# Performance work log

Hardware: AMD Instinct MI355X
Metric: run time of the kernel (lower is better)

## Reference

```python
import jax, jax.numpy as jnp
import numpy as np

B, S, D, H = 2, 2048, 2048, 16
DK = D // H
THETA = 10000.0


def setup_inputs() -> dict:
    key = jax.random.key(0)
    ks = jax.random.split(key, 5)
    scale = 0.02
    return {
        "x": jax.random.normal(ks[0], (B, S, D), dtype=jnp.float32),
        "W_Q": jax.random.normal(ks[1], (D, D), dtype=jnp.float32) * scale,
        "W_K": jax.random.normal(ks[2], (D, D), dtype=jnp.float32) * scale,
        "W_V": jax.random.normal(ks[3], (D, D), dtype=jnp.float32) * scale,
        "W_O": jax.random.normal(ks[4], (D, D), dtype=jnp.float32) * scale,
        "token_positions": jnp.arange(S, dtype=jnp.int32),
    }


def _rope(x, pos):
    # x: [B, S, H, DK]; pos: [S]. Interleaved-pair rotation (cs336 RoPE).
    half = DK // 2
    inv_freq = THETA ** (-(jnp.arange(half, dtype=jnp.float32) / half))  # [half]
    ang = pos.astype(jnp.float32)[:, None] * inv_freq[None, :]           # [S, half]
    cos = jnp.cos(ang)[None, :, None, :]                                 # [1,S,1,half]
    sin = jnp.sin(ang)[None, :, None, :]
    x1, x2 = x[..., ::2], x[..., 1::2]
    r1 = x1 * cos - x2 * sin
    r2 = x1 * sin + x2 * cos
    return jnp.stack([r1, r2], axis=-1).reshape(x.shape)


def reference(x, W_Q, W_K, W_V, W_O, token_positions):
    # QKV projections (Linear with no bias: y = x @ W^T)
    Q = (x @ W_Q.T).reshape(B, S, H, DK)
    K = (x @ W_K.T).reshape(B, S, H, DK)
    V = (x @ W_V.T).reshape(B, S, H, DK)
    Q = _rope(Q, token_positions)
    K = _rope(K, token_positions)
    scores = jnp.einsum("bqhd,bkhd->bhqk", Q, K) / jnp.sqrt(jnp.float32(DK))
    causal = jnp.tril(jnp.ones((S, S), dtype=bool))  # True = attend
    scores = jnp.where(causal[None, None], scores, -jnp.inf)
    attn = jax.nn.softmax(scores, axis=-1)
    out = jnp.einsum("bhqk,bkhd->bqhd", attn, V).reshape(B, S, D)
    return out @ W_O.T
```

## Files before the change

kernel.cpp:

```cpp
#include <hip/hip_runtime.h>
#include <hip/hip_bf16.h>
#include <cstdint>
#include <cstddef>

#define B_ 2
#define S_ 2048
#define D_ 2048
#define H_ 16
#define DK_ 128
#define M_ (B_*S_)

typedef __attribute__((ext_vector_type(8))) __bf16 bf16x8;
typedef __attribute__((ext_vector_type(4))) float f32x4;
typedef __attribute__((ext_vector_type(16))) float f32x16;

__device__ __forceinline__ unsigned short f2bf(float f) {
  union { float f; unsigned int u; } v; v.f = f;
  unsigned int r = (v.u + 0x7fffu + ((v.u >> 16) & 1u)) >> 16;
  return (unsigned short)r;
}
__device__ __forceinline__ float bf2f(unsigned short b) {
  union { unsigned int u; float f; } v; v.u = ((unsigned int)b) << 16;
  return v.f;
}

__device__ __forceinline__ void gld16(const void* g, void* l) {
  __builtin_amdgcn_global_load_lds(
      (const __attribute__((address_space(1))) unsigned int*)g,
      (__attribute__((address_space(3))) unsigned int*)l, 16, 0, 0);
}

__global__ void cvt_bf16(const float* __restrict__ src, unsigned short* __restrict__ dst, int n) {
  int i = (blockIdx.x * blockDim.x + threadIdx.x) * 4;
  if (i + 3 < n) {
    float4 v = *(const float4*)(src + i);
    dst[i+0] = f2bf(v.x); dst[i+1] = f2bf(v.y);
    dst[i+2] = f2bf(v.z); dst[i+3] = f2bf(v.w);
  }
}

template<int WRITE_BF16>
__global__ __launch_bounds__(256) void gemm_bt(const unsigned short* __restrict__ A,
                                               const unsigned short* __restrict__ W0,
                                               const unsigned short* __restrict__ W1,
                                               const unsigned short* __restrict__ W2,
                                               void* __restrict__ C0, void* __restrict__ C1,
                                               void* __restrict__ C2,
                                               int M, int N, int K) {
  __shared__ unsigned short sA[128 * 32];
  __shared__ unsigned short sB[128 * 32];
  const int z = blockIdx.z;
  const unsigned short* Bt = (z == 0) ? W0 : (z == 1) ? W1 : W2;
  void* Cout = (z == 0) ? C0 : (z == 1) ? C1 : C2;

  const int tid  = threadIdx.x;
  const int lane = tid & 63;
  const int wid  = tid >> 6;
  const int wm = wid >> 1, wn = wid & 1;
  const int quad = lane >> 4, l16 = lane & 15;
  const int bm = blockIdx.y * 128, bn = blockIdx.x * 128;
  const int srow = lane >> 2;
  const int scol = (lane & 3) * 8;

  f32x4 acc[4][4];
  #pragma unroll
  for (int i = 0; i < 4; ++i)
    #pragma unroll
    for (int j = 0; j < 4; ++j)
      acc[i][j] = (f32x4){0.f, 0.f, 0.f, 0.f};

  for (int k0 = 0; k0 < K; k0 += 32) {
    __syncthreads();
    #pragma unroll
    for (int p = 0; p < 2; ++p) {
      int row = p * 64 + wid * 16;
      gld16(A  + (size_t)(bm + row + srow) * K + k0 + scol, sA + row * 32);
      gld16(Bt + (size_t)(bn + row + srow) * K + k0 + scol, sB + row * 32);
    }
    __syncthreads();

    bf16x8 af[4], bfr[4];
    #pragma unroll
    for (int i = 0; i < 4; ++i)
      af[i] = *(const bf16x8*)(sA + (wm * 64 + i * 16 + l16) * 32 + quad * 8);
    #pragma unroll
    for (int j = 0; j < 4; ++j)
      bfr[j] = *(const bf16x8*)(sB + (wn * 64 + j * 16 + l16) * 32 + quad * 8);
    #pragma unroll
    for (int i = 0; i < 4; ++i)
      #pragma unroll
      for (int j = 0; j < 4; ++j)
        acc[i][j] = __builtin_amdgcn_mfma_f32_16x16x32_bf16(af[i], bfr[j], acc[i][j], 0, 0, 0);
  }

  #pragma unroll
  for (int i = 0; i < 4; ++i) {
    int row = bm + wm * 64 + i * 16 + quad * 4;
    #pragma unroll
    for (int j = 0; j < 4; ++j) {
      int col = bn + wn * 64 + j * 16 + l16;
      #pragma unroll
      for (int r = 0; r < 4; ++r) {
        if (WRITE_BF16)
          ((unsigned short*)Cout)[(size_t)(row + r) * N + col] = f2bf(acc[i][j][r]);
        else
          ((float*)Cout)[(size_t)(row + r) * N + col] = acc[i][j][r];
      }
    }
  }
}

__global__ void rope_kernel(unsigned short* __restrict__ Q, unsigned short* __restrict__ K,
                            const int* __restrict__ pos) {
  int idx = blockIdx.x * blockDim.x + threadIdx.x;
  int i = idx & 63;
  int h = (idx >> 6) & (H_ - 1);
  int s = (idx >> 10) & (S_ - 1);
  int b = idx >> 21;
  float p = (float)pos[s];
  float inv = expf(-(float)i * (9.210340371976184f / 64.0f));
  float ang = p * inv;
  float sn, cs;
  sincosf(ang, &sn, &cs);
  size_t base = (((size_t)b * S_ + s) * D_) + (size_t)h * DK_ + 2 * i;
  float x1 = bf2f(Q[base]), x2 = bf2f(Q[base + 1]);
  Q[base]     = f2bf(x1 * cs - x2 * sn);
  Q[base + 1] = f2bf(x1 * sn + x2 * cs);
  x1 = bf2f(K[base]); x2 = bf2f(K[base + 1]);
  K[base]     = f2bf(x1 * cs - x2 * sn);
  K[base + 1] = f2bf(x1 * sn + x2 * cs);
}

__global__ __launch_bounds__(256) void transpose_bf16(const unsigned short* __restrict__ src,
                                                      unsigned short* __restrict__ dst) {
  __shared__ unsigned short sT[64 * 64];
  const int b = blockIdx.y;
  const int tx = blockIdx.x & 31, ty = blockIdx.x >> 5;
  const size_t base = (size_t)b * 2048 * 2048;
  const int m0 = ty * 64, c0 = tx * 64;
  const int tid = threadIdx.x;
  #pragma unroll
  for (int c = 0; c < 2; ++c) {
    int idx = tid + c * 256;
    int row = idx >> 3;
    int chk = idx & 7;
    uint4 v = *(const uint4*)(src + base + (size_t)(m0 + row) * 2048 + c0 + chk * 8);
    *(uint4*)(sT + row * 64 + ((chk ^ (row & 7)) * 8)) = v;
  }
  __syncthreads();
  #pragma unroll
  for (int c = 0; c < 2; ++c) {
    int idx = tid + c * 256;
    int orow = idx >> 3;
    int ocol = (idx & 7) * 8;
    unsigned short tmp[8];
    #pragma unroll
    for (int j = 0; j < 8; ++j) {
      int lr = ocol + j;
      int lc = orow;
      tmp[j] = sT[lr * 64 + (((lc >> 3) ^ (lr & 7)) * 8) + (lc & 7)];
    }
    *(uint4*)(dst + base + (size_t)(c0 + orow) * 2048 + m0 + ocol) = *(const uint4*)tmp;
  }
}

__global__ __launch_bounds__(256, 2) void flash_attn(const unsigned short* __restrict__ Q,
                                                     const unsigned short* __restrict__ K,
                                                     const unsigned short* __restrict__ VT,
                                                     unsigned short* __restrict__ O) {
  __shared__ unsigned short sK[2][64 * 128];
  __shared__ unsigned short sVT[2][128 * 64];
  __shared__ unsigned short sP[4][32 * 64];

  const int tid = threadIdx.x, lane = tid & 63, wid = tid >> 6;
  const int half = lane >> 5, l32 = lane & 31;
  const int qi = 15 - (blockIdx.x & 15);
  const int bh = blockIdx.x >> 4;
  const int h = bh & (H_ - 1), b = bh >> 4;
  const int qw = qi * 128 + wid * 32;
  const size_t qkbase = ((size_t)b * S_) * D_ + (size_t)h * DK_;
  const unsigned short* Qg = Q + qkbase;
  const unsigned short* Kg = K + qkbase;
  const unsigned short* VTg = VT + (size_t)bh * DK_ * S_;
  unsigned short* Og = O + qkbase;
  unsigned short* sPw = sP[wid];

  const int kKeySub = lane >> 4;
  const int kPhys   = lane & 15;
  const int vFeatSub = lane >> 3;
  const int vPhys    = lane & 7;

  bf16x8 qf[8];
  #pragma unroll
  for (int ks = 0; ks < 8; ++ks)
    qf[ks] = *(const bf16x8*)(Qg + (size_t)(qw + l32) * D_ + ks * 16 + half * 8);

  union { unsigned short u[8]; bf16x8 v; } onesu;
  #pragma unroll
  for (int j = 0; j < 8; ++j) onesu.u[j] = 0x3F80;
  const bf16x8 ones = onesu.v;

  f32x16 Oacc[4];
  #pragma unroll
  for (int ft = 0; ft < 4; ++ft)
    #pragma unroll
    for (int r = 0; r < 16; ++r) Oacc[ft][r] = 0.f;
  f32x16 l_acc;
  #pragma unroll
  for (int r = 0; r < 16; ++r) l_acc[r] = 0.f;
  const float scale = 0.08838834764831845f;

  const int nkb = 2 * (qi + 1);

  auto stage = [&](int kb) {
    const int k0 = kb * 64;
    unsigned short* bK = sK[kb & 1];
    unsigned short* bV = sVT[kb & 1];
    #pragma unroll
    for (int p = 0; p < 4; ++p) {
      int issue = wid * 4 + p;
      int key = issue * 4 + kKeySub;
      int logiK = (kPhys & 8) | ((kPhys ^ key) & 7);
      gld16(Kg + (size_t)(k0 + key) * D_ + logiK * 8, bK + issue * 512);
      int feat = issue * 8 + vFeatSub;
      int logiV = vPhys ^ (feat & 7);
      gld16(VTg + (size_t)feat * S_ + k0 + logiV * 8, bV + issue * 512);
    }
  };

  stage(0);

  for (int kb = 0; kb < nkb; ++kb) {
    __syncthreads();
    if (kb + 1 < nkb) stage(kb + 1);

    const int k0 = kb * 64;
    if (k0 > qw + 31) continue;

    const unsigned short* bK = sK[kb & 1];
    const unsigned short* bV = sVT[kb & 1];

    f32x16 sc[2];
    #pragma unroll
    for (int t = 0; t < 2; ++t)
      #pragma unroll
      for (int r = 0; r < 16; ++r) sc[t][r] = 0.f;
    #pragma unroll
    for (int ks = 0; ks < 8; ++ks) {
      const int logi = ks * 2 + half;
      #pragma unroll
      for (int t = 0; t < 2; ++t) {
        const int key = t * 32 + l32;
        const int phys = (logi & 8) | ((logi ^ key) & 7);
        bf16x8 kf = *(const bf16x8*)(bK + key * 128 + phys * 8);
        sc[t] = __builtin_amdgcn_mfma_f32_32x32x16_bf16(qf[ks], kf, sc[t], 0, 0, 0);
      }
    }

    const bool diag = (k0 + 63 > qw);
    #pragma unroll
    for (int t = 0; t < 2; ++t) {
      const int col = t * 32 + l32;
      const int keyg = k0 + col;
      #pragma unroll
      for (int r = 0; r < 16; ++r) {
        const int rl = (r & 3) + 8 * (r >> 2) + 4 * half;
        float v = sc[t][r] * scale;
        if (diag && (keyg > qw + rl)) v = -1e30f;
        sPw[rl * 64 + (((col >> 3) ^ (rl & 7)) * 8) + (col & 7)] = f2bf(__expf(v));
      }
    }

    #pragma unroll
    for (int ksp = 0; ksp < 4; ++ksp) {
      const int logi = ksp * 2 + half;
      bf16x8 pf = *(const bf16x8*)(sPw + l32 * 64 + ((logi ^ (l32 & 7)) * 8));
      l_acc = __builtin_amdgcn_mfma_f32_32x32x16_bf16(pf, ones, l_acc, 0, 0, 0);
      #pragma unroll
      for (int ft = 0; ft < 4; ++ft) {
        const int feat = ft * 32 + l32;
        const int phys = logi ^ (feat & 7);
        bf16x8 vf = *(const bf16x8*)(bV + feat * 64 + phys * 8);
        Oacc[ft] = __builtin_amdgcn_mfma_f32_32x32x16_bf16(pf, vf, Oacc[ft], 0, 0, 0);
      }
    }
  }

  #pragma unroll
  for (int ft = 0; ft < 4; ++ft) {
    const int feat = ft * 32 + l32;
    #pragma unroll
    for (int r = 0; r < 16; ++r) {
      const int rl = (r & 3) + 8 * (r >> 2) + 4 * half;
      Og[(size_t)(qw + rl) * D_ + feat] = f2bf(Oacc[ft][r] / l_acc[r]);
    }
  }
}

extern "C" void kernel_launch(void* const* d_in, const int* in_sizes, int n_in,
                              void* d_out, int out_size, void* d_ws, size_t ws_size,
                              hipStream_t stream) {
  const float* x  = (const float*)d_in[0];
  const float* Wq = (const float*)d_in[1];
  const float* Wk = (const float*)d_in[2];
  const float* Wv = (const float*)d_in[3];
  const float* Wo = (const float*)d_in[4];
  const int*  pos = (const int*)d_in[5];
  float* out = (float*)d_out;

  char* ws = (char*)d_ws;
  size_t off = 0;
  auto alloc = [&](size_t bytes) { void* p = ws + off; off += (bytes + 255) & ~255ULL; return p; };
  const size_t nx = (size_t)M_ * D_;
  const size_t nw = (size_t)D_ * D_;
  unsigned short* xb  = (unsigned short*)alloc(nx * 2);
  unsigned short* wqb = (unsigned short*)alloc(nw * 2);
  unsigned short* wkb = (unsigned short*)alloc(nw * 2);
  unsigned short* wvb = (unsigned short*)alloc(nw * 2);
  unsigned short* wob = (unsigned short*)alloc(nw * 2);
  unsigned short* Qb  = (unsigned short*)alloc(nx * 2);
  unsigned short* Kb  = (unsigned short*)alloc(nx * 2);
  unsigned short* Vb  = (unsigned short*)alloc(nx * 2);
  unsigned short* AOb = xb;
  unsigned short* VTb = wqb;

  hipLaunchKernelGGL(cvt_bf16, dim3(nx / 1024), dim3(256), 0, stream, x,  xb,  (int)nx);
  hipLaunchKernelGGL(cvt_bf16, dim3(nw / 1024), dim3(256), 0, stream, Wq, wqb, (int)nw);
  hipLaunchKernelGGL(cvt_bf16, dim3(nw / 1024), dim3(256), 0, stream, Wk, wkb, (int)nw);
  hipLaunchKernelGGL(cvt_bf16, dim3(nw / 1024), dim3(256), 0, stream, Wv, wvb, (int)nw);
  hipLaunchKernelGGL(cvt_bf16, dim3(nw / 1024), dim3(256), 0, stream, Wo, wob, (int)nw);

  hipLaunchKernelGGL((gemm_bt<1>), dim3(D_ / 128, M_ / 128, 3), dim3(256), 0, stream,
                     xb, wqb, wkb, wvb, (void*)Qb, (void*)Kb, (void*)Vb, M_, D_, D_);

  hipLaunchKernelGGL(rope_kernel, dim3((B_ * S_ * H_ * 64) / 256), dim3(256), 0, stream, Qb, Kb, pos);

  hipLaunchKernelGGL(transpose_bf16, dim3(1024, 2), dim3(256), 0, stream, Vb, VTb);

  hipLaunchKernelGGL(flash_attn, dim3(B_ * H_ * (S_ / 128)), dim3(256), 0, stream, Qb, Kb, VTb, AOb);

  hipLaunchKernelGGL((gemm_bt<0>), dim3(D_ / 128, M_ / 128, 1), dim3(256), 0, stream,
                     AOb, wob, wob, wob, (void*)out, (void*)out, (void*)out, M_, D_, D_);
}
```

Before: 459.9 us.

## Fuse conversions, double-buffer GEMM LDS, read V directly from global in attention

```diff
diff --git a/kernel.cpp b/kernel.cpp
--- a/kernel.cpp
+++ b/kernel.cpp
@@ -30,13 +30,26 @@
       (__attribute__((address_space(3))) unsigned int*)l, 16, 0, 0);
 }
 
-__global__ void cvt_bf16(const float* __restrict__ src, unsigned short* __restrict__ dst, int n) {
-  int i = (blockIdx.x * blockDim.x + threadIdx.x) * 4;
-  if (i + 3 < n) {
-    float4 v = *(const float4*)(src + i);
-    dst[i+0] = f2bf(v.x); dst[i+1] = f2bf(v.y);
-    dst[i+2] = f2bf(v.z); dst[i+3] = f2bf(v.w);
-  }
+__global__ __launch_bounds__(256) void cvt_all(const float* __restrict__ x,
+                                               const float* __restrict__ wq, const float* __restrict__ wk,
+                                               const float* __restrict__ wv, const float* __restrict__ wo,
+                                               unsigned short* __restrict__ xb,
+                                               unsigned short* __restrict__ wqb, unsigned short* __restrict__ wkb,
+                                               unsigned short* __restrict__ wvb, unsigned short* __restrict__ wob) {
+  const size_t NX = (size_t)M_ * D_;
+  size_t i = ((size_t)blockIdx.x * 256 + threadIdx.x) * 4;
+  const float* src; unsigned short* dst; size_t o;
+  if (i < NX) { src = x; dst = xb; o = i; }
+  else {
+    size_t j = i - NX;
+    int w = (int)(j >> 22);
+    o = j & ((1u << 22) - 1);
+    src = (w == 0) ? wq : (w == 1) ? wk : (w == 2) ? wv : wo;
+    dst = (w == 0) ? wqb : (w == 1) ? wkb : (w == 2) ? wvb : wob;
+  }
+  float4 v = *(const float4*)(src + o);
+  dst[o+0] = f2bf(v.x); dst[o+1] = f2bf(v.y);
+  dst[o+2] = f2bf(v.z); dst[o+3] = f2bf(v.w);
 }
 
 template<int WRITE_BF16>
@@ -47,8 +60,8 @@
                                                void* __restrict__ C0, void* __restrict__ C1,
                                                void* __restrict__ C2,
                                                int M, int N, int K) {
-  __shared__ unsigned short sA[128 * 32];
-  __shared__ unsigned short sB[128 * 32];
+  __shared__ unsigned short sA[2][128 * 32];
+  __shared__ unsigned short sB[2][128 * 32];
   const int z = blockIdx.z;
   const unsigned short* Bt = (z == 0) ? W0 : (z == 1) ? W1 : W2;
   void* Cout = (z == 0) ? C0 : (z == 1) ? C1 : C2;
@@ -69,23 +82,31 @@
     for (int j = 0; j < 4; ++j)
       acc[i][j] = (f32x4){0.f, 0.f, 0.f, 0.f};
 
-  for (int k0 = 0; k0 < K; k0 += 32) {
-    __syncthreads();
+  auto stage = [&](int kb) {
+    const int k0 = kb * 32;
     #pragma unroll
     for (int p = 0; p < 2; ++p) {
       int row = p * 64 + wid * 16;
-      gld16(A  + (size_t)(bm + row + srow) * K + k0 + scol, sA + row * 32);
-      gld16(Bt + (size_t)(bn + row + srow) * K + k0 + scol, sB + row * 32);
-    }
+      gld16(A  + (size_t)(bm + row + srow) * K + k0 + scol, sA[kb & 1] + row * 32);
+      gld16(Bt + (size_t)(bn + row + srow) * K + k0 + scol, sB[kb & 1] + row * 32);
+    }
+  };
+
+  const int nk = K / 32;
+  stage(0);
+  for (int kb = 0; kb < nk; ++kb) {
     __syncthreads();
-
+    if (kb + 1 < nk) stage(kb + 1);
+
+    const unsigned short* cA = sA[kb & 1];
+    const unsigned short* cB = sB[kb & 1];
     bf16x8 af[4], bfr[4];
     #pragma unroll
     for (int i = 0; i < 4; ++i)
-      af[i] = *(const bf16x8*)(sA + (wm * 64 + i * 16 + l16) * 32 + quad * 8);
+      af[i] = *(const bf16x8*)(cA + (wm * 64 + i * 16 + l16) * 32 + quad * 8);
     #pragma unroll
     for (int j = 0; j < 4; ++j)
-      bfr[j] = *(const bf16x8*)(sB + (wn * 64 + j * 16 + l16) * 32 + quad * 8);
+      bfr[j] = *(const bf16x8*)(cB + (wn * 64 + j * 16 + l16) * 32 + quad * 8);
     #pragma unroll
     for (int i = 0; i < 4; ++i)
       #pragma unroll
@@ -164,12 +185,11 @@
   }
 }
 
-__global__ __launch_bounds__(256, 2) void flash_attn(const unsigned short* __restrict__ Q,
+__global__ __launch_bounds__(256, 3) void flash_attn(const unsigned short* __restrict__ Q,
                                                      const unsigned short* __restrict__ K,
                                                      const unsigned short* __restrict__ VT,
                                                      unsigned short* __restrict__ O) {
   __shared__ unsigned short sK[2][64 * 128];
-  __shared__ unsigned short sVT[2][128 * 64];
   __shared__ unsigned short sP[4][32 * 64];
 
   const int tid = threadIdx.x, lane = tid & 63, wid = tid >> 6;
@@ -187,8 +207,6 @@
 
   const int kKeySub = lane >> 4;
   const int kPhys   = lane & 15;
-  const int vFeatSub = lane >> 3;
-  const int vPhys    = lane & 7;
 
   bf16x8 qf[8];
   #pragma unroll
@@ -215,16 +233,12 @@
   auto stage = [&](int kb) {
     const int k0 = kb * 64;
     unsigned short* bK = sK[kb & 1];
-    unsigned short* bV = sVT[kb & 1];
     #pragma unroll
     for (int p = 0; p < 4; ++p) {
       int issue = wid * 4 + p;
       int key = issue * 4 + kKeySub;
       int logiK = (kPhys & 8) | ((kPhys ^ key) & 7);
       gld16(Kg + (size_t)(k0 + key) * D_ + logiK * 8, bK + issue * 512);
-      int feat = issue * 8 + vFeatSub;
-      int logiV = vPhys ^ (feat & 7);
-      gld16(VTg + (size_t)feat * S_ + k0 + logiV * 8, bV + issue * 512);
     }
   };
 
@@ -238,36 +252,28 @@
     if (k0 > qw + 31) continue;
 
     const unsigned short* bK = sK[kb & 1];
-    const unsigned short* bV = sVT[kb & 1];
-
-    f32x16 sc[2];
-    #pragma unroll
-    for (int t = 0; t < 2; ++t)
-      #pragma unroll
-      for (int r = 0; r < 16; ++r) sc[t][r] = 0.f;
-    #pragma unroll
-    for (int ks = 0; ks < 8; ++ks) {
-      const int logi = ks * 2 + half;
-      #pragma unroll
-      for (int t = 0; t < 2; ++t) {
-        const int key = t * 32 + l32;
+    const bool diag = (k0 + 63 > qw);
+
+    #pragma unroll
+    for (int t = 0; t < 2; ++t) {
+      f32x16 sc;
+      #pragma unroll
+      for (int r = 0; r < 16; ++r) sc[r] = 0.f;
+      const int key = t * 32 + l32;
+      #pragma unroll
+      for (int ks = 0; ks < 8; ++ks) {
+        const int logi = ks * 2 + half;
         const int phys = (logi & 8) | ((logi ^ key) & 7);
         bf16x8 kf = *(const bf16x8*)(bK + key * 128 + phys * 8);
-        sc[t] = __builtin_amdgcn_mfma_f32_32x32x16_bf16(qf[ks], kf, sc[t], 0, 0, 0);
+        sc = __builtin_amdgcn_mfma_f32_32x32x16_bf16(qf[ks], kf, sc, 0, 0, 0);
       }
-    }
-
-    const bool diag = (k0 + 63 > qw);
-    #pragma unroll
-    for (int t = 0; t < 2; ++t) {
-      const int col = t * 32 + l32;
-      const int keyg = k0 + col;
+      const int keyg = k0 + key;
       #pragma unroll
       for (int r = 0; r < 16; ++r) {
         const int rl = (r & 3) + 8 * (r >> 2) + 4 * half;
-        float v = sc[t][r] * scale;
+        float v = sc[r] * scale;
         if (diag && (keyg > qw + rl)) v = -1e30f;
-        sPw[rl * 64 + (((col >> 3) ^ (rl & 7)) * 8) + (col & 7)] = f2bf(__expf(v));
+        sPw[rl * 64 + (((key >> 3) ^ (rl & 7)) * 8) + (key & 7)] = f2bf(__expf(v));
       }
     }
 
@@ -279,8 +285,7 @@
       #pragma unroll
       for (int ft = 0; ft < 4; ++ft) {
         const int feat = ft * 32 + l32;
-        const int phys = logi ^ (feat & 7);
-        bf16x8 vf = *(const bf16x8*)(bV + feat * 64 + phys * 8);
+        bf16x8 vf = *(const bf16x8*)(VTg + (size_t)feat * S_ + k0 + logi * 8);
         Oacc[ft] = __builtin_amdgcn_mfma_f32_32x32x16_bf16(pf, vf, Oacc[ft], 0, 0, 0);
       }
     }
@@ -324,11 +329,8 @@
   unsigned short* AOb = xb;
   unsigned short* VTb = wqb;
 
-  hipLaunchKernelGGL(cvt_bf16, dim3(nx / 1024), dim3(256), 0, stream, x,  xb,  (int)nx);
-  hipLaunchKernelGGL(cvt_bf16, dim3(nw / 1024), dim3(256), 0, stream, Wq, wqb, (int)nw);
-  hipLaunchKernelGGL(cvt_bf16, dim3(nw / 1024), dim3(256), 0, stream, Wk, wkb, (int)nw);
-  hipLaunchKernelGGL(cvt_bf16, dim3(nw / 1024), dim3(256), 0, stream, Wv, wvb, (int)nw);
-  hipLaunchKernelGGL(cvt_bf16, dim3(nw / 1024), dim3(256), 0, stream, Wo, wob, (int)nw);
+  hipLaunchKernelGGL(cvt_all, dim3((nx + 4 * nw) / 1024), dim3(256), 0, stream,
+                     x, Wq, Wk, Wv, Wo, xb, wqb, wkb, wvb, wob);
 
   hipLaunchKernelGGL((gemm_bt<1>), dim3(D_ / 128, M_ / 128, 3), dim3(256), 0, stream,
                      xb, wqb, wkb, wvb, (void*)Qb, (void*)Kb, (void*)Vb, M_, D_, D_);
```

Measured after the change: 920.2 us. 100% more time.
